# Performance work log

Measured on AMD Instinct MI355X. Metric: run time of the kernel, lower is better.

The kernel has to match this reference:

```python
import jax, jax.numpy as jnp
import numpy as np

B, T, D, H = 4, 2048, 1024, 16
HD = D // H


def setup_inputs() -> dict:
    key = jax.random.key(0)
    ks = jax.random.split(key, 10)
    s = 1.0 / np.sqrt(D)
    # xavier_uniform bound for wbias [T,T]: sqrt(6/(T+T))
    wb_bound = float(np.sqrt(6.0 / (T + T)))
    return {
        "x": jax.random.normal(ks[0], (B, T, D), dtype=jnp.float32),
        "Wq": jax.random.normal(ks[1], (D, D), dtype=jnp.float32) * s,
        "bq": jnp.zeros((D,), dtype=jnp.float32),
        "Wk": jax.random.normal(ks[2], (D, D), dtype=jnp.float32) * s,
        "bk": jnp.zeros((D,), dtype=jnp.float32),
        "Wv": jax.random.normal(ks[3], (D, D), dtype=jnp.float32) * s,
        "bv": jnp.zeros((D,), dtype=jnp.float32),
        "Wo": jax.random.normal(ks[4], (D, D), dtype=jnp.float32) * s,
        "bo": jnp.zeros((D,), dtype=jnp.float32),
        "wbias": jax.random.uniform(ks[5], (T, T), dtype=jnp.float32,
                                    minval=-wb_bound, maxval=wb_bound),
    }


def reference(x, Wq, bq, Wk, bk, Wv, bv, Wo, bo, wbias):
    Bc, Tc, Dc = x.shape
    # projections, split heads: [B, H, T, HD]
    def proj(W, b):
        y = x @ W + b
        return y.reshape(Bc, Tc, H, HD).transpose(0, 2, 1, 3)

    Q = proj(Wq, bq)
    K = proj(Wk, bk)
    V = proj(Wv, bv)

    Q_sig = jax.nn.sigmoid(Q)
    eK = jnp.exp(K)                      # [B,H,T,HD]
    ew = jnp.exp(wbias[:Tc, :Tc])        # [T,T]

    num = jnp.einsum('ts,bhsd->bhtd', ew, eK * V)
    den = jnp.einsum('ts,bhsd->bhtd', ew, eK)
    out = Q_sig * (num / den)            # [B,H,T,HD]

    out = out.transpose(0, 2, 1, 3).reshape(Bc, Tc, Dc)
    return out @ Wo + bo
```

## Files before the change

kernel.cpp:

```cpp
#include <hip/hip_runtime.h>
#include <hip/hip_bf16.h>


#define AS1(p) ((const __attribute__((address_space(1))) void*)(p))
#define AS3(p) ((__attribute__((address_space(3))) void*)(p))

typedef _Float16 half8 __attribute__((ext_vector_type(8)));
typedef _Float16 half4v __attribute__((ext_vector_type(4)));
typedef float floatx16 __attribute__((ext_vector_type(16)));
typedef int intx4 __attribute__((ext_vector_type(4)));
typedef int intx8 __attribute__((ext_vector_type(8)));

__device__ __forceinline__ long frag_off(int r, int k) {
  return (long)(((((r >> 5) * 4 + (k >> 4)) * 2 + ((k >> 3) & 1)) * 32 + (r & 31)) * 8 + (k & 7));
}
__device__ __forceinline__ long off8(int r, int k) {
  return (long)((((((r >> 5) * 2 + ((k >> 6) & 1)) * 2 + ((k >> 4) & 1)) * 2 + ((k >> 5) & 1)) * 32 +
                 (r & 31)) * 16 + (k & 15));
}

__global__ __launch_bounds__(256) void prep_all(
    const float* __restrict__ x, const float* __restrict__ wb, const float* __restrict__ Wq,
    const float* __restrict__ Wk, const float* __restrict__ Wv, const float* __restrict__ Wo,
    _Float16* __restrict__ x_h, char* __restrict__ E8, _Float16* __restrict__ WqkvT,
    _Float16* __restrict__ WoT) {
  __shared__ _Float16 lds[64 * 132];
  const int bid = blockIdx.x;
  const int tid = threadIdx.x;

  if (bid < 1024) {
    const int tm = bid >> 4, tk = bid & 15;
    const long tbase = (long)bid * 8192;
#pragma unroll
    for (int p = 0; p < 4; ++p) {
      const int s = p * 256 + tid;
      const int r = ((s >> 8) << 5) + (s & 31);
      const int k = ((s >> 6) & 3) * 16 + ((s >> 5) & 1) * 8;
      const float* sp = x + (long)(tm * 128 + r) * 1024 + tk * 64 + k;
      const float4 v0 = *(const float4*)sp;
      const float4 v1 = *(const float4*)(sp + 4);
      half8 h;
      h[0] = (_Float16)v0.x; h[1] = (_Float16)v0.y; h[2] = (_Float16)v0.z; h[3] = (_Float16)v0.w;
      h[4] = (_Float16)v1.x; h[5] = (_Float16)v1.y; h[6] = (_Float16)v1.z; h[7] = (_Float16)v1.w;
      *(half8*)(x_h + tbase + (long)s * 8) = h;
    }
    return;
  }

  if (bid >= 1536) {
    const int e = bid - 1536;
    const int tt = e >> 4, ts = e & 15;
    char* dst = E8 + (long)e * 16384;
#pragma unroll
    for (int p = 0; p < 16; ++p) {
      const int idx = p * 256 + tid;
      const int r = idx >> 5, k = (idx & 31) * 4;
      const float4 v = *(const float4*)(wb + (long)(tt * 128 + r) * 2048 + ts * 128 + k);
      const float e0 = (__expf(v.x) - 1.0f) * 32.0f, e1 = (__expf(v.y) - 1.0f) * 32.0f;
      const float e2 = (__expf(v.z) - 1.0f) * 32.0f, e3 = (__expf(v.w) - 1.0f) * 32.0f;
      int pk = __builtin_amdgcn_cvt_pk_fp8_f32(e0, e1, 0, false);
      pk = __builtin_amdgcn_cvt_pk_fp8_f32(e2, e3, pk, true);
      *(int*)(dst + off8(r, k)) = pk;
    }
    return;
  }

  const int b2 = bid - 1024;
  const float* src0;
  const float* src1 = nullptr;
  _Float16* dst;
  int tn, tk, cb = 0;
  if (b2 < 128) {
    tn = b2 >> 4; tk = b2 & 15; src0 = Wq; dst = WqkvT;
  } else if (b2 < 384) {
    const int t = b2 - 128;
    tn = 8 + (t >> 4); tk = t & 15; cb = (tn - 8) * 64; src0 = Wk; src1 = Wv; dst = WqkvT;
  } else {
    const int t = b2 - 384;
    tn = t >> 4; tk = t & 15; src0 = Wo; dst = WoT;
  }
  if (!src1) {
#pragma unroll
    for (int p = 0; p < 8; ++p) {
      const int kl = p * 8 + (tid >> 5);
      const int cl = (tid & 31) * 4;
      const float4 v = *(const float4*)(src0 + (long)(tk * 64 + kl) * 1024 + tn * 128 + cl);
      half4v h;
      h[0] = (_Float16)v.x; h[1] = (_Float16)v.y; h[2] = (_Float16)v.z; h[3] = (_Float16)v.w;
      *(half4v*)(lds + kl * 132 + cl) = h;
    }
  } else {
#pragma unroll
    for (int m = 0; m < 2; ++m) {
      const float* s = m ? src1 : src0;
      const int rb = m ? 32 : 0;
#pragma unroll
      for (int p = 0; p < 4; ++p) {
        const int kl = p * 16 + (tid >> 4);
        const int cl = (tid & 15) * 4;
        const int rl = (cl >> 5) * 64 + rb + (cl & 31);
        const float4 v = *(const float4*)(s + (long)(tk * 64 + kl) * 1024 + cb + cl);
        half4v h;
        h[0] = (_Float16)v.x; h[1] = (_Float16)v.y; h[2] = (_Float16)v.z; h[3] = (_Float16)v.w;
        *(half4v*)(lds + kl * 132 + rl) = h;
      }
    }
  }
  __syncthreads();
  const long tbase = (long)(tn * 16 + tk) * 8192;
#pragma unroll
  for (int p = 0; p < 4; ++p) {
    const int s = p * 256 + tid;
    const int r = ((s >> 8) << 5) + (s & 31);
    const int kl = ((s >> 6) & 3) * 16 + ((s >> 5) & 1) * 8;
    half8 h;
#pragma unroll
    for (int j = 0; j < 8; ++j) h[j] = lds[(kl + j) * 132 + r];
    *(half8*)(dst + tbase + (long)s * 8) = h;
  }
}

template <int VM, bool STAGE, bool RDNEXT>
__device__ __forceinline__ void aft_p(int g, const _Float16* __restrict__ Ablk,
                                      const _Float16* __restrict__ Bblk, _Float16* ring,
                                      int tid, int wid, int lane, int wm, int wn,
                                      half8 (&curA)[2][2], half8 (&curB)[2][2],
                                      half8 (&nxtA)[2][2], half8 (&nxtB)[2][2],
                                      floatx16 (&acc)[2][2]) {
  if (STAGE) {
    const int gs = g + 3;
    const int t = gs >> 1;
    const long goff = (long)(tid >> 7) * 2048 + (gs & 1) * 1024 + (tid & 127) * 8;
    _Float16* dA = ring + (gs & 3) * 4096 + wid * 512;
    _Float16* dB = ring + 16384 + (gs & 3) * 8192 + wid * 512;
    __builtin_amdgcn_global_load_lds(AS1(Ablk + (long)t * 8192 + goff), AS3(dA), 16, 0, 0);
    __builtin_amdgcn_global_load_lds(AS1(Bblk + (long)t * 8192 + goff), AS3(dB), 16, 0, 0);
    __builtin_amdgcn_global_load_lds(AS1(Bblk + (long)(16 + t) * 8192 + goff), AS3(dB + 4096),
                                     16, 0, 0);
  }
  if constexpr (VM >= 0) {
    asm volatile("s_waitcnt vmcnt(%0) lgkmcnt(0)" ::"i"(VM) : "memory");
    __builtin_amdgcn_s_barrier();
  }
  if (RDNEXT) {
    const _Float16* sA = ring + ((g + 1) & 3) * 4096 + lane * 8;
    const _Float16* sB = ring + 16384 + ((g + 1) & 3) * 8192 + lane * 8;
#pragma unroll
    for (int mt = 0; mt < 2; ++mt)
#pragma unroll
      for (int ks = 0; ks < 2; ++ks)
        nxtA[mt][ks] = *(const half8*)(sA + (((wm >> 5) + mt) * 2 + ks) * 512);
#pragma unroll
    for (int nt = 0; nt < 2; ++nt)
#pragma unroll
      for (int ks = 0; ks < 2; ++ks)
        nxtB[nt][ks] = *(const half8*)(sB + (((wn >> 5) + nt) * 2 + ks) * 512);
  }
  __builtin_amdgcn_s_setprio(1);
#pragma unroll
  for (int ks = 0; ks < 2; ++ks)
#pragma unroll
    for (int mt = 0; mt < 2; ++mt)
#pragma unroll
      for (int nt = 0; nt < 2; ++nt)
        acc[mt][nt] =
            __builtin_amdgcn_mfma_f32_32x32x16_f16(curA[mt][ks], curB[nt][ks], acc[mt][nt], 0, 0, 0);
  __builtin_amdgcn_s_setprio(0);
}

template <int MODE>
__global__ __launch_bounds__(512, 2) void gemm_bt2(
    const _Float16* __restrict__ A, const _Float16* __restrict__ Bt, void* __restrict__ Cv,
    const float* __restrict__ bias0, const float* __restrict__ bias1,
    const float* __restrict__ bias2, char* __restrict__ Zt8, float* __restrict__ cs) {
  __shared__ __align__(16) _Float16 ring[49152];
  const int tid = threadIdx.x;
  const int wid = tid >> 6, lane = tid & 63;
  const int l32 = lane & 31, khalf = lane >> 5;

  const int f = blockIdx.x;
  const int j = f >> 3;
  const int bxs = (f & 7) * 8 + (j & 7);
  const int bys = j >> 3;
  const int m0 = bxs * 128, n0 = bys * 256;
  const int wm = (wid >> 2) * 64, wn = (wid & 3) * 64;

  const _Float16* Ablk = A + (long)bxs * 131072;
  const _Float16* Bblk = Bt + (long)(bys * 2) * 131072;

#pragma unroll
  for (int g0 = 0; g0 < 3; ++g0) {
    const int t = g0 >> 1;
    const long goff = (long)(tid >> 7) * 2048 + (g0 & 1) * 1024 + (tid & 127) * 8;
    __builtin_amdgcn_global_load_lds(AS1(Ablk + (long)t * 8192 + goff),
                                     AS3(ring + g0 * 4096 + wid * 512), 16, 0, 0);
    __builtin_amdgcn_global_load_lds(AS1(Bblk + (long)t * 8192 + goff),
                                     AS3(ring + 16384 + g0 * 8192 + wid * 512), 16, 0, 0);
    __builtin_amdgcn_global_load_lds(AS1(Bblk + (long)(16 + t) * 8192 + goff),
                                     AS3(ring + 16384 + g0 * 8192 + 4096 + wid * 512), 16, 0, 0);
  }
  asm volatile("s_waitcnt vmcnt(6)" ::: "memory");
  __builtin_amdgcn_s_barrier();
  asm volatile("" ::: "memory");

  half8 fA0[2][2], fB0[2][2], fA1[2][2], fB1[2][2];
  {
    const _Float16* sA = ring + lane * 8;
    const _Float16* sB = ring + 16384 + lane * 8;
#pragma unroll
    for (int mt = 0; mt < 2; ++mt)
#pragma unroll
      for (int ks = 0; ks < 2; ++ks)
        fA0[mt][ks] = *(const half8*)(sA + (((wm >> 5) + mt) * 2 + ks) * 512);
#pragma unroll
    for (int nt = 0; nt < 2; ++nt)
#pragma unroll
      for (int ks = 0; ks < 2; ++ks)
        fB0[nt][ks] = *(const half8*)(sB + (((wn >> 5) + nt) * 2 + ks) * 512);
  }

  floatx16 acc[2][2] = {};
#pragma unroll
  for (int gb = 0; gb < 28; gb += 2) {
    aft_p<6, true, true>(gb + 0, Ablk, Bblk, ring, tid, wid, lane, wm, wn, fA0, fB0, fA1, fB1, acc);
    aft_p<6, true, true>(gb + 1, Ablk, Bblk, ring, tid, wid, lane, wm, wn, fA1, fB1, fA0, fB0, acc);
  }
  aft_p<6, true, true>(28, Ablk, Bblk, ring, tid, wid, lane, wm, wn, fA0, fB0, fA1, fB1, acc);
  aft_p<3, false, true>(29, Ablk, Bblk, ring, tid, wid, lane, wm, wn, fA1, fB1, fA0, fB0, acc);
  aft_p<0, false, true>(30, Ablk, Bblk, ring, tid, wid, lane, wm, wn, fA0, fB0, fA1, fB1, acc);
  aft_p<-1, false, false>(31, Ablk, Bblk, ring, tid, wid, lane, wm, wn, fA1, fB1, fA0, fB0, acc);

  if (MODE == 0) {
    if (n0 < 1024) {
      _Float16* Qs = (_Float16*)Cv;
#pragma unroll
      for (int mt = 0; mt < 2; ++mt) {
        const long ttile = (m0 + wm + mt * 32) >> 5;
#pragma unroll
        for (int nt = 0; nt < 2; ++nt) {
          const int col = n0 + wn + nt * 32 + l32;
          const float bb = bias0[col];
          const long base = (ttile * 32 + (((n0 + wn) >> 5) + nt)) * 1024;
#pragma unroll
          for (int q = 0; q < 4; ++q) {
            half4v o;
#pragma unroll
            for (int rr = 0; rr < 4; ++rr) {
              const float v = acc[mt][nt][q * 4 + rr] + bb;
              o[rr] = (_Float16)(1.0f / (1.0f + __expf(-v)));
            }
            *(half4v*)(Qs + base + q * 256 + lane * 4) = o;
          }
        }
      }
    } else {
      const int grp = (n0 - 1024 + wn) >> 6;
      const int ch = grp * 32 + l32;
      const float bkc = bias1[ch], bvc = bias2[ch];
      const int jn = grp * 64 + l32;
      const int b = m0 >> 11;
      char* Z8 = Zt8 + (long)b * 4194304 +
                 ((long)(jn >> 7) * 16 + ((m0 & 2047) >> 7)) * 16384;
      const int jnl = jn & 127;
      float sk = 0.f, sz = 0.f;
#pragma unroll
      for (int mt = 0; mt < 2; ++mt) {
#pragma unroll
        for (int q = 0; q < 4; ++q) {
          float ekv[4], ekk[4];
#pragma unroll
          for (int rr = 0; rr < 4; ++rr) {
            const float ek = __expf(acc[mt][0][q * 4 + rr] + bkc);
            const float vv = acc[mt][1][q * 4 + rr] + bvc;
            ekk[rr] = ek;
            ekv[rr] = ek * vv;
            sk += ek;
            sz += ek * vv;
          }
          const int sl = wm + mt * 32 + 4 * khalf + 8 * q;
          int pn = __builtin_amdgcn_cvt_pk_fp8_f32(ekv[0] * 0.25f, ekv[1] * 0.25f, 0, false);
          pn = __builtin_amdgcn_cvt_pk_fp8_f32(ekv[2] * 0.25f, ekv[3] * 0.25f, pn, true);
          int pd = __builtin_amdgcn_cvt_pk_fp8_f32(ekk[0] * 0.25f, ekk[1] * 0.25f, 0, false);
          pd = __builtin_amdgcn_cvt_pk_fp8_f32(ekk[2] * 0.25f, ekk[3] * 0.25f, pd, true);
          *(int*)(Z8 + off8(jnl, sl)) = pn;
          *(int*)(Z8 + off8(jnl + 32, sl)) = pd;
        }
      }
      atomicAdd(&cs[(long)b * 2048 + ch * 2], sz);
      atomicAdd(&cs[(long)b * 2048 + ch * 2 + 1], sk);
    }
    return;
  }

#pragma unroll
  for (int mt = 0; mt < 2; ++mt)
#pragma unroll
    for (int nt = 0; nt < 2; ++nt) {
      const int col = n0 + wn + nt * 32 + l32;
      const float bb = bias0[col];
#pragma unroll
      for (int reg = 0; reg < 16; ++reg) {
        const int row = m0 + wm + mt * 32 + 4 * khalf + 8 * (reg >> 2) + (reg & 3);
        ((float*)Cv)[(long)row * 1024 + col] = acc[mt][nt][reg] + bb;
      }
    }
}

template <int VM, bool STAGE, int SLOT>
__device__ __forceinline__ void g2_phase(int g, char* __restrict__ ringA, char* __restrict__ ringB,
                                         const char* At0, const char* At1,
                                         const char* Bt0, const char* Bt1,
                                         int tid, int lane, int wm, int wn,
                                         floatx16 (&acc)[2][4]) {
  const int l32 = lane & 31, khalf = lane >> 5;
  intx8 a8[2], b8[4];
#pragma unroll
  for (int mt = 0; mt < 2; ++mt) {
    const int G = (wm >> 5) + mt;
    const char* pa = ringA + SLOT * 16384 + (G >> 2) * 8192 + (G & 3) * 2048 + khalf * 512 + l32 * 16;
    const intx4 alo = *(const intx4*)pa;
    const intx4 ahi = *(const intx4*)(pa + 1024);
    a8[mt] = __builtin_shufflevector(alo, ahi, 0, 1, 2, 3, 4, 5, 6, 7);
  }
#pragma unroll
  for (int nt = 0; nt < 4; ++nt) {
    const int Gn = (wn >> 5) + nt;
    const char* pb = ringB + SLOT * 16384 + (Gn >> 2) * 8192 + (Gn & 3) * 2048 + khalf * 512 + l32 * 16;
    const intx4 blo = *(const intx4*)pb;
    const intx4 bhi = *(const intx4*)(pb + 1024);
    b8[nt] = __builtin_shufflevector(blo, bhi, 0, 1, 2, 3, 4, 5, 6, 7);
  }
  if (STAGE) {
    const int ks = g + 2;
    constexpr int SS = (SLOT + 2) % 3;
    const long gsrc = (long)(ks >> 1) * 16384 + (long)(tid >> 7) * 4096 + (long)(ks & 1) * 2048 +
                      (tid & 127) * 16;
    char* dA = ringA + SS * 16384 + tid * 16;
    char* dB = ringB + SS * 16384 + tid * 16;
    __builtin_amdgcn_global_load_lds(AS1(At0 + gsrc), AS3(dA), 16, 0, 0);
    __builtin_amdgcn_global_load_lds(AS1(At1 + gsrc), AS3(dA + 8192), 16, 0, 0);
    __builtin_amdgcn_global_load_lds(AS1(Bt0 + gsrc), AS3(dB), 16, 0, 0);
    __builtin_amdgcn_global_load_lds(AS1(Bt1 + gsrc), AS3(dB + 8192), 16, 0, 0);
  }
  if constexpr (VM >= 0) {
    asm volatile("s_waitcnt vmcnt(%0)" ::"i"(VM) : "memory");
    __builtin_amdgcn_s_barrier();
  }
  asm volatile("s_waitcnt lgkmcnt(0)" ::: "memory");
  __builtin_amdgcn_s_setprio(1);
#pragma unroll
  for (int mt = 0; mt < 2; ++mt)
#pragma unroll
    for (int nt = 0; nt < 4; ++nt)
      acc[mt][nt] = __builtin_amdgcn_mfma_scale_f32_32x32x64_f8f6f4(
          a8[mt], b8[nt], acc[mt][nt], 0, 0, 0, 127u, 0, 127u);
  __builtin_amdgcn_s_setprio(0);
  if constexpr (VM >= 0) {
    __builtin_amdgcn_s_barrier();
    asm volatile("" ::: "memory");
  }
}

__global__ __launch_bounds__(512, 1) void gemm2_fp8(
    const char* __restrict__ E8, const char* __restrict__ Zt8, _Float16* __restrict__ OH,
    const _Float16* __restrict__ Qsig, const float* __restrict__ cs) {
  __shared__ __align__(16) char ring[98304];
  char* ringA = ring;
  char* ringB = ring + 49152;
  const int tid = threadIdx.x;
  const int wid = tid >> 6, lane = tid & 63;
  const int l32 = lane & 31, khalf = lane >> 5;

  const int f = blockIdx.x;
  const int bxs = f & 7;
  const int bys = (f >> 3) & 7;
  const int bzs = f >> 6;
  const int m0 = bxs * 256;
  const int wm = (wid >> 1) * 64, wn = (wid & 1) * 128;

  const char* At0 = E8 + (long)(bxs * 2) * 262144;
  const char* At1 = At0 + 262144;
  const char* Bt0 = Zt8 + (long)bzs * 4194304 + (long)(bys * 2) * 262144;
  const char* Bt1 = Bt0 + 262144;

#pragma unroll
  for (int ks = 0; ks < 2; ++ks) {
    const long gsrc = (long)(tid >> 7) * 4096 + (long)(ks & 1) * 2048 + (tid & 127) * 16;
    char* dA = ringA + ks * 16384 + tid * 16;
    char* dB = ringB + ks * 16384 + tid * 16;
    __builtin_amdgcn_global_load_lds(AS1(At0 + gsrc), AS3(dA), 16, 0, 0);
    __builtin_amdgcn_global_load_lds(AS1(At1 + gsrc), AS3(dA + 8192), 16, 0, 0);
    __builtin_amdgcn_global_load_lds(AS1(Bt0 + gsrc), AS3(dB), 16, 0, 0);
    __builtin_amdgcn_global_load_lds(AS1(Bt1 + gsrc), AS3(dB + 8192), 16, 0, 0);
  }
  asm volatile("s_waitcnt vmcnt(4)" ::: "memory");
  __builtin_amdgcn_s_barrier();
  asm volatile("" ::: "memory");

  floatx16 acc[2][4] = {};
#pragma unroll 1
  for (int gb = 0; gb < 30; gb += 3) {
    g2_phase<4, true, 0>(gb + 0, ringA, ringB, At0, At1, Bt0, Bt1, tid, lane, wm, wn, acc);
    g2_phase<4, true, 1>(gb + 1, ringA, ringB, At0, At1, Bt0, Bt1, tid, lane, wm, wn, acc);
    g2_phase<4, true, 2>(gb + 2, ringA, ringB, At0, At1, Bt0, Bt1, tid, lane, wm, wn, acc);
  }
  g2_phase<0, false, 0>(30, ringA, ringB, At0, At1, Bt0, Bt1, tid, lane, wm, wn, acc);
  g2_phase<-1, false, 1>(31, ringA, ringB, At0, At1, Bt0, Bt1, tid, lane, wm, wn, acc);

  const int g32b = bys * 4 + (wn >> 6);
#pragma unroll
  for (int mt = 0; mt < 2; ++mt) {
    const long ttile = (long)(bzs * 2048 + m0 + wm + mt * 32) >> 5;
#pragma unroll
    for (int p = 0; p < 2; ++p) {
      const int g32 = g32b + p;
      const int ch = g32 * 32 + l32;
      const float2 c2 = *(const float2*)(cs + (long)bzs * 2048 + ch * 2);
      const long qbase = (ttile * 32 + g32) * 1024;
#pragma unroll
      for (int q = 0; q < 4; ++q) {
        const half4v qv = *(const half4v*)(Qsig + qbase + q * 256 + lane * 4);
#pragma unroll
        for (int rr = 0; rr < 4; ++rr) {
          const int reg = q * 4 + rr;
          const float num = c2.x + acc[mt][2 * p][reg] * 0.125f;
          const float den = c2.y + acc[mt][2 * p + 1][reg] * 0.125f;
          const int r = m0 + wm + mt * 32 + 4 * khalf + 8 * q + rr;
          const int R = bzs * 2048 + r;
          const long off = ((long)(R >> 7) * 16 + (ch >> 6)) * 8192 + frag_off(R & 127, ch & 63);
          OH[off] = (_Float16)((float)qv[rr] * num / den);
        }
      }
    }
  }
}

extern "C" void kernel_launch(void* const* d_in, const int* in_sizes, int n_in, void* d_out,
                              int out_size, void* d_ws, size_t ws_size, hipStream_t stream) {
  const float* x = (const float*)d_in[0];
  const float* Wq = (const float*)d_in[1];
  const float* bq = (const float*)d_in[2];
  const float* Wk = (const float*)d_in[3];
  const float* bk = (const float*)d_in[4];
  const float* Wv = (const float*)d_in[5];
  const float* bv = (const float*)d_in[6];
  const float* Wo = (const float*)d_in[7];
  const float* bo = (const float*)d_in[8];
  const float* wb = (const float*)d_in[9];

  char* ws = (char*)d_ws;
  _Float16* x_h = (_Float16*)(ws + 0);
  _Float16* WqkvT = (_Float16*)(ws + 16777216);
  _Float16* WoT = (_Float16*)(ws + 23068672);
  char* E8 = (char*)(ws + 25165824);
  _Float16* Qsig = (_Float16*)(ws + 29360128);
  char* Zt8 = (char*)(ws + 46137344);
  _Float16* OutHead = (_Float16*)(ws + 62914560);
  float* cs = (float*)(ws + 79691776);

  hipMemsetAsync(cs, 0, 4 * 2048 * sizeof(float), stream);

  prep_all<<<1792, 256, 0, stream>>>(x, wb, Wq, Wk, Wv, Wo, x_h, E8, WqkvT, WoT);

  gemm_bt2<0><<<768, 512, 0, stream>>>(x_h, WqkvT, Qsig, bq, bk, bv, Zt8, cs);

  gemm2_fp8<<<256, 512, 0, stream>>>(E8, Zt8, OutHead, Qsig, cs);

  gemm_bt2<2><<<256, 512, 0, stream>>>(OutHead, WoT, d_out, bo, nullptr, nullptr, nullptr, nullptr);
}
```

Baseline: 250.1 us.

## Load GEMM B fragments directly from global into registers, shrink LDS ring

The GEMM no longer stages the B operand through LDS. Each wave loads its own B fragments straight from global memory into registers one step ahead, and only A goes through the LDS ring, which shrinks from 96KB to 32KB. The barrier and wait move to after the MFMAs, with adjusted vmcnt values. This cuts LDS traffic and footprint and may raise occupancy, at the cost of redundant global/L2 reads of B across waves and exposed global latency on the register loads.

Measured after the change: 253.5 us. No clear change (+1.4%).

```diff
diff --git a/kernel.cpp b/kernel.cpp
--- a/kernel.cpp
+++ b/kernel.cpp
@@ -120,41 +120,33 @@
   }
 }
 
-template <int VM, bool STAGE, bool RDNEXT>
-__device__ __forceinline__ void aft_p(int g, const _Float16* __restrict__ Ablk,
-                                      const _Float16* __restrict__ Bblk, _Float16* ring,
-                                      int tid, int wid, int lane, int wm, int wn,
-                                      half8 (&curA)[2][2], half8 (&curB)[2][2],
-                                      half8 (&nxtA)[2][2], half8 (&nxtB)[2][2],
-                                      floatx16 (&acc)[2][2]) {
+template <int VM, bool STAGE, bool LDB, bool RDN, bool BAR>
+__device__ __forceinline__ void aft_p(
+    int g, const _Float16* __restrict__ Ablk, const _Float16* __restrict__ Bf0,
+    const _Float16* __restrict__ Bf1, _Float16* ring, long thrA, int wid, int lane, int wm,
+    half8 (&aCur)[2][2], half8 (&aNxt)[2][2], half8 (&bCur)[2][2], half8 (&bNxt)[2][2],
+    floatx16 (&acc)[2][2]) {
+  if (RDN) {
+    const _Float16* sA = ring + ((g + 1) & 3) * 4096 + lane * 8;
+#pragma unroll
+    for (int mt = 0; mt < 2; ++mt)
+#pragma unroll
+      for (int ks = 0; ks < 2; ++ks)
+        aNxt[mt][ks] = *(const half8*)(sA + (((wm >> 5) + mt) * 2 + ks) * 512);
+  }
+  if (LDB) {
+    const long gb = (long)((g + 1) >> 1) * 8192 + (long)((g + 1) & 1) * 1024;
+#pragma unroll
+    for (int ks = 0; ks < 2; ++ks) {
+      bNxt[0][ks] = *(const half8*)(Bf0 + gb + ks * 512);
+      bNxt[1][ks] = *(const half8*)(Bf1 + gb + ks * 512);
+    }
+  }
   if (STAGE) {
     const int gs = g + 3;
-    const int t = gs >> 1;
-    const long goff = (long)(tid >> 7) * 2048 + (gs & 1) * 1024 + (tid & 127) * 8;
-    _Float16* dA = ring + (gs & 3) * 4096 + wid * 512;
-    _Float16* dB = ring + 16384 + (gs & 3) * 8192 + wid * 512;
-    __builtin_amdgcn_global_load_lds(AS1(Ablk + (long)t * 8192 + goff), AS3(dA), 16, 0, 0);
-    __builtin_amdgcn_global_load_lds(AS1(Bblk + (long)t * 8192 + goff), AS3(dB), 16, 0, 0);
-    __builtin_amdgcn_global_load_lds(AS1(Bblk + (long)(16 + t) * 8192 + goff), AS3(dB + 4096),
-                                     16, 0, 0);
-  }
-  if constexpr (VM >= 0) {
-    asm volatile("s_waitcnt vmcnt(%0) lgkmcnt(0)" ::"i"(VM) : "memory");
-    __builtin_amdgcn_s_barrier();
-  }
-  if (RDNEXT) {
-    const _Float16* sA = ring + ((g + 1) & 3) * 4096 + lane * 8;
-    const _Float16* sB = ring + 16384 + ((g + 1) & 3) * 8192 + lane * 8;
-#pragma unroll
-    for (int mt = 0; mt < 2; ++mt)
-#pragma unroll
-      for (int ks = 0; ks < 2; ++ks)
-        nxtA[mt][ks] = *(const half8*)(sA + (((wm >> 5) + mt) * 2 + ks) * 512);
-#pragma unroll
-    for (int nt = 0; nt < 2; ++nt)
-#pragma unroll
-      for (int ks = 0; ks < 2; ++ks)
-        nxtB[nt][ks] = *(const half8*)(sB + (((wn >> 5) + nt) * 2 + ks) * 512);
+    const long go = (long)(gs >> 1) * 8192 + (long)(gs & 1) * 1024 + thrA;
+    __builtin_amdgcn_global_load_lds(AS1(Ablk + go), AS3(ring + (gs & 3) * 4096 + wid * 512), 16,
+                                     0, 0);
   }
   __builtin_amdgcn_s_setprio(1);
 #pragma unroll
@@ -164,8 +156,13 @@
 #pragma unroll
       for (int nt = 0; nt < 2; ++nt)
         acc[mt][nt] =
-            __builtin_amdgcn_mfma_f32_32x32x16_f16(curA[mt][ks], curB[nt][ks], acc[mt][nt], 0, 0, 0);
+            __builtin_amdgcn_mfma_f32_32x32x16_f16(aCur[mt][ks], bCur[nt][ks], acc[mt][nt], 0, 0, 0);
   __builtin_amdgcn_s_setprio(0);
+  if (BAR) {
+    asm volatile("s_waitcnt vmcnt(%0)" ::"i"(VM < 0 ? 0 : VM) : "memory");
+    __builtin_amdgcn_s_barrier();
+    asm volatile("" ::: "memory");
+  }
 }
 
 template <int MODE>
@@ -173,7 +170,7 @@
     const _Float16* __restrict__ A, const _Float16* __restrict__ Bt, void* __restrict__ Cv,
     const float* __restrict__ bias0, const float* __restrict__ bias1,
     const float* __restrict__ bias2, char* __restrict__ Zt8, float* __restrict__ cs) {
-  __shared__ __align__(16) _Float16 ring[49152];
+  __shared__ __align__(16) _Float16 ring[16384];
   const int tid = threadIdx.x;
   const int wid = tid >> 6, lane = tid & 63;
   const int l32 = lane & 31, khalf = lane >> 5;
@@ -188,47 +185,51 @@
   const _Float16* Ablk = A + (long)bxs * 131072;
   const _Float16* Bblk = Bt + (long)(bys * 2) * 131072;
 
+  const int c0 = wn, c1 = wn + 32;
+  const _Float16* Bf0 = Bblk + (long)(c0 >> 7) * 131072 + ((c0 & 127) >> 5) * 2048 + lane * 8;
+  const _Float16* Bf1 = Bblk + (long)(c1 >> 7) * 131072 + ((c1 & 127) >> 5) * 2048 + lane * 8;
+
+  const long thrA = (long)(tid >> 7) * 2048 + (tid & 127) * 8;
+
 #pragma unroll
   for (int g0 = 0; g0 < 3; ++g0) {
-    const int t = g0 >> 1;
-    const long goff = (long)(tid >> 7) * 2048 + (g0 & 1) * 1024 + (tid & 127) * 8;
-    __builtin_amdgcn_global_load_lds(AS1(Ablk + (long)t * 8192 + goff),
-                                     AS3(ring + g0 * 4096 + wid * 512), 16, 0, 0);
-    __builtin_amdgcn_global_load_lds(AS1(Bblk + (long)t * 8192 + goff),
-                                     AS3(ring + 16384 + g0 * 8192 + wid * 512), 16, 0, 0);
-    __builtin_amdgcn_global_load_lds(AS1(Bblk + (long)(16 + t) * 8192 + goff),
-                                     AS3(ring + 16384 + g0 * 8192 + 4096 + wid * 512), 16, 0, 0);
-  }
-  asm volatile("s_waitcnt vmcnt(6)" ::: "memory");
+    const long go = (long)(g0 >> 1) * 8192 + (long)(g0 & 1) * 1024 + thrA;
+    __builtin_amdgcn_global_load_lds(AS1(Ablk + go), AS3(ring + g0 * 4096 + wid * 512), 16, 0, 0);
+  }
+  half8 a0[2][2], a1[2][2], b0[2][2], b1[2][2];
+#pragma unroll
+  for (int ks = 0; ks < 2; ++ks) {
+    b0[0][ks] = *(const half8*)(Bf0 + ks * 512);
+    b0[1][ks] = *(const half8*)(Bf1 + ks * 512);
+  }
+  asm volatile("s_waitcnt vmcnt(0)" ::: "memory");
   __builtin_amdgcn_s_barrier();
   asm volatile("" ::: "memory");
-
-  half8 fA0[2][2], fB0[2][2], fA1[2][2], fB1[2][2];
   {
     const _Float16* sA = ring + lane * 8;
-    const _Float16* sB = ring + 16384 + lane * 8;
 #pragma unroll
     for (int mt = 0; mt < 2; ++mt)
 #pragma unroll
       for (int ks = 0; ks < 2; ++ks)
-        fA0[mt][ks] = *(const half8*)(sA + (((wm >> 5) + mt) * 2 + ks) * 512);
-#pragma unroll
-    for (int nt = 0; nt < 2; ++nt)
-#pragma unroll
-      for (int ks = 0; ks < 2; ++ks)
-        fB0[nt][ks] = *(const half8*)(sB + (((wn >> 5) + nt) * 2 + ks) * 512);
+        a0[mt][ks] = *(const half8*)(sA + (((wm >> 5) + mt) * 2 + ks) * 512);
   }
 
   floatx16 acc[2][2] = {};
 #pragma unroll
-  for (int gb = 0; gb < 28; gb += 2) {
-    aft_p<6, true, true>(gb + 0, Ablk, Bblk, ring, tid, wid, lane, wm, wn, fA0, fB0, fA1, fB1, acc);
-    aft_p<6, true, true>(gb + 1, Ablk, Bblk, ring, tid, wid, lane, wm, wn, fA1, fB1, fA0, fB0, acc);
-  }
-  aft_p<6, true, true>(28, Ablk, Bblk, ring, tid, wid, lane, wm, wn, fA0, fB0, fA1, fB1, acc);
-  aft_p<3, false, true>(29, Ablk, Bblk, ring, tid, wid, lane, wm, wn, fA1, fB1, fA0, fB0, acc);
-  aft_p<0, false, true>(30, Ablk, Bblk, ring, tid, wid, lane, wm, wn, fA0, fB0, fA1, fB1, acc);
-  aft_p<-1, false, false>(31, Ablk, Bblk, ring, tid, wid, lane, wm, wn, fA1, fB1, fA0, fB0, acc);
+  for (int pr = 0; pr < 14; ++pr) {
+    aft_p<5, true, true, true, true>(2 * pr, Ablk, Bf0, Bf1, ring, thrA, wid, lane, wm,
+                                     a0, a1, b0, b1, acc);
+    aft_p<5, true, true, true, true>(2 * pr + 1, Ablk, Bf0, Bf1, ring, thrA, wid, lane, wm,
+                                     a1, a0, b1, b0, acc);
+  }
+  aft_p<5, true, true, true, true>(28, Ablk, Bf0, Bf1, ring, thrA, wid, lane, wm,
+                                   a0, a1, b0, b1, acc);
+  aft_p<4, false, true, true, true>(29, Ablk, Bf0, Bf1, ring, thrA, wid, lane, wm,
+                                    a1, a0, b1, b0, acc);
+  aft_p<-1, false, true, true, false>(30, Ablk, Bf0, Bf1, ring, thrA, wid, lane, wm,
+                                      a0, a1, b0, b1, acc);
+  aft_p<-1, false, false, false, false>(31, Ablk, Bf0, Bf1, ring, thrA, wid, lane, wm,
+                                        a1, a0, b1, b0, acc);
 
   if (MODE == 0) {
     if (n0 < 1024) {
```
